# Kernel optimization log

Measured on AMD Instinct MI355X. Metric: run time of the kernel, lower is better.

Reference implementation:

```python
import jax, jax.numpy as jnp
import numpy as np

N = 500_000   # nodes
E = 16_000_000  # edges (avg degree 32)


def setup_inputs() -> dict:
    key = jax.random.key(0)
    ks = jax.random.split(key, 12)
    x = jax.random.normal(ks[0], (N, 1), dtype=jnp.float32)
    edge_index = jax.random.randint(ks[1], (2, E), 0, N, dtype=jnp.int32)
    # GCNConv weights: conv1(1->4), conv2(4->4), conv3(4->2), classifier Linear(2->1)
    def w(k, fin, fout):
        return jax.random.normal(k, (fin, fout), dtype=jnp.float32) / np.sqrt(fin)
    W1, b1 = w(ks[2], 1, 4), jnp.zeros((4,), jnp.float32)
    W2, b2 = w(ks[3], 4, 4), jnp.zeros((4,), jnp.float32)
    W3, b3 = w(ks[4], 4, 2), jnp.zeros((2,), jnp.float32)
    Wc, bc = w(ks[5], 2, 1), jnp.zeros((1,), jnp.float32)
    return {"x": x, "edge_index": edge_index, "W1": W1, "b1": b1,
            "W2": W2, "b2": b2, "W3": W3, "b3": b3, "Wc": Wc, "bc": bc}


def _gcn_conv(h, src, dst, dinv, W, b):
    # PyG GCNConv: out = D^{-1/2}(A+I)D^{-1/2} (h W) + b
    h = h @ W  # [N, Fout], tiny Fout so transform-first is cheapest
    norm = dinv[src] * dinv[dst]          # [E]
    msg = h[src] * norm[:, None]          # [E, Fout]
    agg = jax.ops.segment_sum(msg, dst, num_segments=N)
    # self-loop contribution: norm = dinv[i]^2
    agg = agg + h * (dinv * dinv)[:, None]
    return agg + b


def reference(x, edge_index, W1, b1, W2, b2, W3, b3, Wc, bc):
    src, dst = edge_index[0], edge_index[1]
    # degree including self-loop (count of incoming edges at dst, PyG gcn_norm)
    deg = jax.ops.segment_sum(jnp.ones((E,), jnp.float32), dst, num_segments=N) + 1.0
    dinv = jax.lax.rsqrt(deg)
    h = jnp.tanh(_gcn_conv(x, src, dst, dinv, W1, b1))
    h = jnp.tanh(_gcn_conv(h, src, dst, dinv, W2, b2))
    h = jnp.tanh(_gcn_conv(h, src, dst, dinv, W3, b3))
    out = h @ Wc + bc
    return (out, h)
```

## Files before the change

kernel.cpp:

```cpp
#include <hip/hip_runtime.h>

#define NN   500000
#define NE   16000000

#define NBUCK   245
#define NWGA    1000
#define CHUNKA4 4000
#define NBINB   1954
#define NWGB    2000
#define CHUNKB4 2000
#define CAP     14336

typedef int      vint4   __attribute__((ext_vector_type(4)));
typedef float    vfloat4 __attribute__((ext_vector_type(4)));
typedef float    vfloat2 __attribute__((ext_vector_type(2)));
typedef _Float16 vhalf4  __attribute__((ext_vector_type(4)));
typedef _Float16 vhalf2  __attribute__((ext_vector_type(2)));

__global__ __launch_bounds__(256) void hist_kernel(const int* __restrict__ dst,
                                                   int* __restrict__ wgHist,
                                                   int shift, int nbin, int chunk4) {
    __shared__ int hist[NBINB];
    for (int i = threadIdx.x; i < nbin; i += 256) hist[i] = 0;
    __syncthreads();
    const vint4* d4 = (const vint4*)(dst + (size_t)blockIdx.x * chunk4 * 4);
    for (int i = threadIdx.x; i < chunk4; i += 256) {
        vint4 d = __builtin_nontemporal_load(d4 + i);
        atomicAdd(&hist[d.x >> shift], 1);
        atomicAdd(&hist[d.y >> shift], 1);
        atomicAdd(&hist[d.z >> shift], 1);
        atomicAdd(&hist[d.w >> shift], 1);
    }
    __syncthreads();
    int* row = wgHist + (size_t)blockIdx.x * nbin;
    for (int i = threadIdx.x; i < nbin; i += 256) row[i] = hist[i];
}

__global__ __launch_bounds__(256) void scanbins_kernel(int* __restrict__ wgHist,
                                                       int* __restrict__ binTotal,
                                                       int nwg, int nbin) {
    __shared__ int partials[256];
    int bin = blockIdx.x;
    int t = threadIdx.x;
    int per = (nwg + 255) / 256;
    int w0 = t * per;
    int w1 = w0 + per; if (w1 > nwg) w1 = nwg;
    int s = 0;
    for (int w = w0; w < w1; ++w) s += wgHist[(size_t)w * nbin + bin];
    partials[t] = s;
    __syncthreads();
    if (t == 0) {
        int run = 0;
        for (int i = 0; i < 256; ++i) { int tmp = partials[i]; partials[i] = run; run += tmp; }
        binTotal[bin] = run;
    }
    __syncthreads();
    int off = partials[t];
    for (int w = w0; w < w1; ++w) {
        size_t idx = (size_t)w * nbin + bin;
        int v = wgHist[idx];
        wgHist[idx] = off;
        off += v;
    }
}

__global__ void scantotal_kernel(const int* __restrict__ binTotal, int* __restrict__ binStart,
                                 int nbin) {
    __shared__ int partials[512];
    int t = threadIdx.x;
    int base = t * 4;
    int v[4]; int s = 0;
#pragma unroll
    for (int j = 0; j < 4; ++j) {
        int b = base + j;
        v[j] = (b < nbin) ? binTotal[b] : 0;
        s += v[j];
    }
    partials[t] = s;
    __syncthreads();
    if (t == 0) {
        int run = 0;
        for (int i = 0; i < 512; ++i) { int tmp = partials[i]; partials[i] = run; run += tmp; }
        binStart[nbin] = run;
    }
    __syncthreads();
    int off = partials[t];
#pragma unroll
    for (int j = 0; j < 4; ++j) {
        int b = base + j;
        if (b < nbin) binStart[b] = off;
        off += v[j];
    }
}

__global__ __launch_bounds__(256) void reorder_kernel(const int* __restrict__ src,
                                                      const int* __restrict__ dst,
                                                      const int* __restrict__ wgHist,
                                                      const int* __restrict__ binStart,
                                                      int* __restrict__ outbuf,
                                                      int shift, int nbin, int chunk4) {
    __shared__ int cur[NBINB];
    const int* row = wgHist + (size_t)blockIdx.x * nbin;
    for (int i = threadIdx.x; i < nbin; i += 256) cur[i] = binStart[i] + row[i];
    __syncthreads();
    const int mask = (1 << shift) - 1;
    const vint4* s4 = (const vint4*)(src + (size_t)blockIdx.x * chunk4 * 4);
    const vint4* d4 = (const vint4*)(dst + (size_t)blockIdx.x * chunk4 * 4);
    for (int i = threadIdx.x; i < chunk4; i += 256) {
        vint4 s = __builtin_nontemporal_load(s4 + i);
        vint4 d = __builtin_nontemporal_load(d4 + i);
        int ss[4] = {s.x, s.y, s.z, s.w};
        int dd[4] = {d.x, d.y, d.z, d.w};
#pragma unroll
        for (int k = 0; k < 4; ++k) {
            int pos = atomicAdd(&cur[dd[k] >> shift], 1);
            outbuf[pos] = (ss[k] << shift) | (dd[k] & mask);
        }
    }
}

__global__ __launch_bounds__(512) void csr_kernel(const int* __restrict__ bktStart,
                                                  const int* __restrict__ bucketbuf,
                                                  int* __restrict__ edgebuf,
                                                  const float* __restrict__ x,
                                                  float* __restrict__ dinv,
                                                  float* __restrict__ p1,
                                                  int* __restrict__ rowStart) {
    __shared__ int cnt[2048];
    __shared__ int pref[2048];
    __shared__ int partials[512];
    int b = blockIdx.x, t = threadIdx.x;
    for (int k = t; k < 2048; k += 512) cnt[k] = 0;
    __syncthreads();
    int e0 = bktStart[b], e1 = bktStart[b + 1];
    int n = e1 - e0;
    for (int i = t; i < n; i += 512)
        atomicAdd(&cnt[bucketbuf[e0 + i] & 2047], 1);
    __syncthreads();
    int base = t * 4;
    int c0 = cnt[base], c1 = cnt[base + 1], c2 = cnt[base + 2], c3 = cnt[base + 3];
    partials[t] = c0 + c1 + c2 + c3;
    __syncthreads();
    if (t == 0) {
        int run = 0;
        for (int i = 0; i < 512; ++i) { int tmp = partials[i]; partials[i] = run; run += tmp; }
    }
    __syncthreads();
    int off = partials[t];
    int cc[4] = {c0, c1, c2, c3};
#pragma unroll
    for (int j = 0; j < 4; ++j) { pref[base + j] = off; off += cc[j]; }
#pragma unroll
    for (int j = 0; j < 4; ++j) {
        int k = base + j;
        int node = b * 2048 + k;
        if (node < NN) {
            rowStart[node] = e0 + pref[k];
            float di = rsqrtf((float)cc[j] + 1.0f);
            dinv[node] = di;
            p1[node] = x[node] * di;
        }
    }
    if (b == NBUCK - 1 && t == 0) rowStart[NN] = e1;
    __syncthreads();
#pragma unroll
    for (int j = 0; j < 4; ++j) { int k = base + j; cnt[k] = e0 + pref[k]; }
    __syncthreads();
    for (int i = t; i < n; i += 512) {
        int e = bucketbuf[e0 + i];
        int pos = atomicAdd(&cnt[e & 2047], 1);
        edgebuf[pos] = e >> 11;
    }
}

__global__ __launch_bounds__(256) void sortbin_kernel(const int* __restrict__ binStart,
                                                      int* __restrict__ edgebuf,
                                                      const float* __restrict__ x,
                                                      float* __restrict__ dinv,
                                                      float* __restrict__ p1,
                                                      int* __restrict__ rowStart) {
    __shared__ int stage[CAP];
    __shared__ int cnt[256];
    __shared__ int pref[256];
    __shared__ int cur[256];
    int b = blockIdx.x, t = threadIdx.x;
    cnt[t] = 0;
    __syncthreads();
    int e0 = binStart[b], e1 = binStart[b + 1];
    int n = e1 - e0;
    if (n > CAP) n = CAP;
    for (int i = t; i < n; i += 256) {
        int e = edgebuf[e0 + i];
        stage[i] = e;
        atomicAdd(&cnt[e & 255], 1);
    }
    __syncthreads();
    if (t == 0) {
        int run = 0;
        for (int i = 0; i < 256; ++i) { pref[i] = run; run += cnt[i]; }
    }
    __syncthreads();
    cur[t] = pref[t];
    int node = b * 256 + t;
    if (node < NN) {
        rowStart[node] = e0 + pref[t];
        float di = rsqrtf((float)cnt[t] + 1.0f);
        dinv[node] = di;
        p1[node] = x[node] * di;
    }
    if (b == NBINB - 1 && t == 0) rowStart[NN] = binStart[NBINB];
    __syncthreads();
    for (int i = t; i < n; i += 256) {
        int e = stage[i];
        int pos = e0 + atomicAdd(&cur[e & 255], 1);
        edgebuf[pos] = e >> 8;
    }
}

__global__ __launch_bounds__(256) void agg1_kernel(const int* __restrict__ rowStart,
                                                   const int* __restrict__ edgebuf,
                                                   const float* __restrict__ p1,
                                                   const float* __restrict__ dinv,
                                                   const float* __restrict__ W1,
                                                   const float* __restrict__ b1,
                                                   const float* __restrict__ W2,
                                                   vhalf4* __restrict__ p2h) {
    int node = blockIdx.x * blockDim.x + threadIdx.x;
    if (node >= NN) return;
    int r0 = rowStart[node], r1 = rowStart[node + 1];
    float s0 = 0.f, s1 = 0.f, s2 = 0.f, s3 = 0.f;
    float s4 = 0.f, s5 = 0.f, s6 = 0.f, s7 = 0.f;
    int k = r0;
    for (; k + 8 <= r1; k += 8) {
        int a = edgebuf[k],     b = edgebuf[k + 1];
        int c = edgebuf[k + 2], d = edgebuf[k + 3];
        int e = edgebuf[k + 4], f = edgebuf[k + 5];
        int g = edgebuf[k + 6], h = edgebuf[k + 7];
        s0 += p1[a]; s1 += p1[b]; s2 += p1[c]; s3 += p1[d];
        s4 += p1[e]; s5 += p1[f]; s6 += p1[g]; s7 += p1[h];
    }
    for (; k < r1; ++k) s0 += p1[edgebuf[k]];
    float acc = ((s0 + s1) + (s2 + s3)) + ((s4 + s5) + (s6 + s7));
    float di = dinv[node];
    float t = di * (acc + p1[node]);
    float h1[4];
#pragma unroll
    for (int f2 = 0; f2 < 4; ++f2) h1[f2] = tanhf(t * W1[f2] + b1[f2]);
    vhalf4 g;
    g.x = (_Float16)(di * (h1[0]*W2[0] + h1[1]*W2[4] + h1[2]*W2[8]  + h1[3]*W2[12]));
    g.y = (_Float16)(di * (h1[0]*W2[1] + h1[1]*W2[5] + h1[2]*W2[9]  + h1[3]*W2[13]));
    g.z = (_Float16)(di * (h1[0]*W2[2] + h1[1]*W2[6] + h1[2]*W2[10] + h1[3]*W2[14]));
    g.w = (_Float16)(di * (h1[0]*W2[3] + h1[1]*W2[7] + h1[2]*W2[11] + h1[3]*W2[15]));
    p2h[node] = g;
}

__global__ __launch_bounds__(256) void agg2_kernel(const int* __restrict__ rowStart,
                                                   const int* __restrict__ edgebuf,
                                                   const vhalf4* __restrict__ p2h,
                                                   const float* __restrict__ dinv,
                                                   const float* __restrict__ b2,
                                                   const float* __restrict__ W3,
                                                   vhalf2* __restrict__ p3h) {
    int node = blockIdx.x * blockDim.x + threadIdx.x;
    if (node >= NN) return;
    int r0 = rowStart[node], r1 = rowStart[node + 1];
    vfloat4 sA = {0.f, 0.f, 0.f, 0.f};
    vfloat4 sB = {0.f, 0.f, 0.f, 0.f};
    vfloat4 sC = {0.f, 0.f, 0.f, 0.f};
    vfloat4 sD = {0.f, 0.f, 0.f, 0.f};
    int k = r0;
    for (; k + 8 <= r1; k += 8) {
        int a = edgebuf[k],     b = edgebuf[k + 1];
        int c = edgebuf[k + 2], d = edgebuf[k + 3];
        int e = edgebuf[k + 4], f = edgebuf[k + 5];
        int g = edgebuf[k + 6], h = edgebuf[k + 7];
        vhalf4 qa = p2h[a], qb = p2h[b], qc = p2h[c], qd = p2h[d];
        vhalf4 qe = p2h[e], qf = p2h[f], qg = p2h[g], qh = p2h[h];
        sA.x += (float)qa.x + (float)qb.x; sB.x += (float)qc.x + (float)qd.x;
        sA.y += (float)qa.y + (float)qb.y; sB.y += (float)qc.y + (float)qd.y;
        sA.z += (float)qa.z + (float)qb.z; sB.z += (float)qc.z + (float)qd.z;
        sA.w += (float)qa.w + (float)qb.w; sB.w += (float)qc.w + (float)qd.w;
        sC.x += (float)qe.x + (float)qf.x; sD.x += (float)qg.x + (float)qh.x;
        sC.y += (float)qe.y + (float)qf.y; sD.y += (float)qg.y + (float)qh.y;
        sC.z += (float)qe.z + (float)qf.z; sD.z += (float)qg.z + (float)qh.z;
        sC.w += (float)qe.w + (float)qf.w; sD.w += (float)qg.w + (float)qh.w;
    }
    for (; k < r1; ++k) {
        vhalf4 q = p2h[edgebuf[k]];
        sA.x += (float)q.x; sA.y += (float)q.y; sA.z += (float)q.z; sA.w += (float)q.w;
    }
    float di = dinv[node];
    vhalf4 pw = p2h[node];
    float h2[4];
    h2[0] = tanhf(di * (sA.x + sB.x + sC.x + sD.x + (float)pw.x) + b2[0]);
    h2[1] = tanhf(di * (sA.y + sB.y + sC.y + sD.y + (float)pw.y) + b2[1]);
    h2[2] = tanhf(di * (sA.z + sB.z + sC.z + sD.z + (float)pw.z) + b2[2]);
    h2[3] = tanhf(di * (sA.w + sB.w + sC.w + sD.w + (float)pw.w) + b2[3]);
    vhalf2 o;
    o.x = (_Float16)(di * (h2[0]*W3[0] + h2[1]*W3[2] + h2[2]*W3[4] + h2[3]*W3[6]));
    o.y = (_Float16)(di * (h2[0]*W3[1] + h2[1]*W3[3] + h2[2]*W3[5] + h2[3]*W3[7]));
    p3h[node] = o;
}

__global__ __launch_bounds__(256) void agg3_kernel(const int* __restrict__ rowStart,
                                                   const int* __restrict__ edgebuf,
                                                   const vhalf2* __restrict__ p3h,
                                                   const float* __restrict__ dinv,
                                                   const float* __restrict__ b3,
                                                   const float* __restrict__ Wc,
                                                   const float* __restrict__ bc,
                                                   float* __restrict__ out) {
    int node = blockIdx.x * blockDim.x + threadIdx.x;
    if (node >= NN) return;
    int r0 = rowStart[node], r1 = rowStart[node + 1];
    float ax = 0.f, ay = 0.f, bx = 0.f, by = 0.f;
    float cx = 0.f, cy = 0.f, dx = 0.f, dy = 0.f;
    int k = r0;
    for (; k + 8 <= r1; k += 8) {
        int a = edgebuf[k],     b = edgebuf[k + 1];
        int c = edgebuf[k + 2], d = edgebuf[k + 3];
        int e = edgebuf[k + 4], f = edgebuf[k + 5];
        int g = edgebuf[k + 6], h = edgebuf[k + 7];
        vhalf2 qa = p3h[a], qb = p3h[b], qc = p3h[c], qd = p3h[d];
        vhalf2 qe = p3h[e], qf = p3h[f], qg = p3h[g], qh = p3h[h];
        ax += (float)qa.x + (float)qb.x; bx += (float)qc.x + (float)qd.x;
        ay += (float)qa.y + (float)qb.y; by += (float)qc.y + (float)qd.y;
        cx += (float)qe.x + (float)qf.x; dx += (float)qg.x + (float)qh.x;
        cy += (float)qe.y + (float)qf.y; dy += (float)qg.y + (float)qh.y;
    }
    for (; k < r1; ++k) {
        vhalf2 q = p3h[edgebuf[k]];
        ax += (float)q.x; ay += (float)q.y;
    }
    float di = dinv[node];
    vhalf2 pw = p3h[node];
    float h0 = tanhf(di * (ax + bx + cx + dx + (float)pw.x) + b3[0]);
    float h1 = tanhf(di * (ay + by + cy + dy + (float)pw.y) + b3[1]);
    __builtin_nontemporal_store(h0 * Wc[0] + h1 * Wc[1] + bc[0], out + node);
    vfloat2 hh; hh.x = h0; hh.y = h1;
    __builtin_nontemporal_store(hh, (vfloat2*)(out + NN) + node);
}


extern "C" void kernel_launch(void* const* d_in, const int* in_sizes, int n_in,
                              void* d_out, int out_size, void* d_ws, size_t ws_size,
                              hipStream_t stream) {
    const float* x   = (const float*)d_in[0];
    const int*   ei  = (const int*)d_in[1];
    const float* W1  = (const float*)d_in[2];
    const float* b1  = (const float*)d_in[3];
    const float* W2  = (const float*)d_in[4];
    const float* b2  = (const float*)d_in[5];
    const float* W3  = (const float*)d_in[6];
    const float* b3  = (const float*)d_in[7];
    const float* Wc  = (const float*)d_in[8];
    const float* bc  = (const float*)d_in[9];
    float* out = (float*)d_out;
    float* ws  = (float*)d_ws;

    const int* src = ei;
    const int* dst = ei + NE;

    float*  dinv     = ws;
    float*  p1       = ws + (size_t)NN;
    vhalf4* p2h      = (vhalf4*)(ws + 2ull * NN);
    vhalf2* p3h      = (vhalf2*)(ws + 4ull * NN);
    int*    rowStart = (int*)(ws + 5ull * NN);
    int*    tail     = (int*)(ws + 6ull * NN + 1);

    const int B = 256;
    const int aggGrid = (NN + B - 1) / B;

    const size_t needA = (6ull * NN + 1 + (size_t)NWGA * NBUCK + NBUCK + NBUCK + 1
                          + 2ull * NE) * 4ull;

    if (ws_size >= needA) {
        int* wgHist    = tail;
        int* bktTotal  = wgHist + (size_t)NWGA * NBUCK;
        int* bktStart  = bktTotal + NBUCK;
        int* bucketbuf = bktStart + NBUCK + 1;
        int* edgebuf   = bucketbuf + (size_t)NE;

        hipLaunchKernelGGL(hist_kernel, dim3(NWGA), dim3(B), 0, stream,
                           dst, wgHist, 11, NBUCK, CHUNKA4);
        hipLaunchKernelGGL(scanbins_kernel, dim3(NBUCK), dim3(B), 0, stream,
                           wgHist, bktTotal, NWGA, NBUCK);
        hipLaunchKernelGGL(scantotal_kernel, dim3(1), dim3(512), 0, stream,
                           bktTotal, bktStart, NBUCK);
        hipLaunchKernelGGL(reorder_kernel, dim3(NWGA), dim3(B), 0, stream,
                           src, dst, wgHist, bktStart, bucketbuf, 11, NBUCK, CHUNKA4);
        hipLaunchKernelGGL(csr_kernel, dim3(NBUCK), dim3(512), 0, stream,
                           bktStart, bucketbuf, edgebuf, x, dinv, p1, rowStart);
        hipLaunchKernelGGL(agg1_kernel, dim3(aggGrid), dim3(B), 0, stream,
                           rowStart, edgebuf, p1, dinv, W1, b1, W2, p2h);
        hipLaunchKernelGGL(agg2_kernel, dim3(aggGrid), dim3(B), 0, stream,
                           rowStart, edgebuf, p2h, dinv, b2, W3, p3h);
        hipLaunchKernelGGL(agg3_kernel, dim3(aggGrid), dim3(B), 0, stream,
                           rowStart, edgebuf, p3h, dinv, b3, Wc, bc, out);
    } else {
        int* wgHist   = tail;
        int* binTotal = wgHist + (size_t)NWGB * NBINB;
        int* binStart = binTotal + NBINB;
        int* edgebuf  = binStart + NBINB + 1;

        hipLaunchKernelGGL(hist_kernel, dim3(NWGB), dim3(B), 0, stream,
                           dst, wgHist, 8, NBINB, CHUNKB4);
        hipLaunchKernelGGL(scanbins_kernel, dim3(NBINB), dim3(B), 0, stream,
                           wgHist, binTotal, NWGB, NBINB);
        hipLaunchKernelGGL(scantotal_kernel, dim3(1), dim3(512), 0, stream,
                           binTotal, binStart, NBINB);
        hipLaunchKernelGGL(reorder_kernel, dim3(NWGB), dim3(B), 0, stream,
                           src, dst, wgHist, binStart, edgebuf, 8, NBINB, CHUNKB4);
        hipLaunchKernelGGL(sortbin_kernel, dim3(NBINB), dim3(B), 0, stream,
                           binStart, edgebuf, x, dinv, p1, rowStart);
        hipLaunchKernelGGL(agg1_kernel, dim3(aggGrid), dim3(B), 0, stream,
                           rowStart, edgebuf, p1, dinv, W1, b1, W2, p2h);
        hipLaunchKernelGGL(agg2_kernel, dim3(aggGrid), dim3(B), 0, stream,
                           rowStart, edgebuf, p2h, dinv, b2, W3, p3h);
        hipLaunchKernelGGL(agg3_kernel, dim3(aggGrid), dim3(B), 0, stream,
                           rowStart, edgebuf, p3h, dinv, b3, Wc, bc, out);
    }
}
```

Before: 738.9 us.

## Split per-bucket CSR build into sub-bin partition plus per-bin sort

Replaces the 245-block csr_kernel, which did a 2048-way shared-memory counting sort per bucket, with two passes. A subbin kernel partitions each bucket into 8 sub-bins of 256 nodes using wave-aggregated ballot atomics. The existing sortbin kernel then finishes the sort with 1954 blocks. This aims to raise parallelism beyond 245 workgroups and cut LDS atomic contention, at the cost of an extra full pass over the 16M-entry edge buffer and one more launch.

```diff
diff --git a/kernel.cpp b/kernel.cpp
--- a/kernel.cpp
+++ b/kernel.cpp
@@ -2,11 +2,11 @@
 
 #define NN   500000
 #define NE   16000000
+#define NBIN 1954
 
 #define NBUCK   245
 #define NWGA    1000
 #define CHUNKA4 4000
-#define NBINB   1954
 #define NWGB    2000
 #define CHUNKB4 2000
 #define CAP     14336
@@ -20,7 +20,7 @@
 __global__ __launch_bounds__(256) void hist_kernel(const int* __restrict__ dst,
                                                    int* __restrict__ wgHist,
                                                    int shift, int nbin, int chunk4) {
-    __shared__ int hist[NBINB];
+    __shared__ int hist[NBIN];
     for (int i = threadIdx.x; i < nbin; i += 256) hist[i] = 0;
     __syncthreads();
     const vint4* d4 = (const vint4*)(dst + (size_t)blockIdx.x * chunk4 * 4);
@@ -99,7 +99,7 @@
                                                       const int* __restrict__ binStart,
                                                       int* __restrict__ outbuf,
                                                       int shift, int nbin, int chunk4) {
-    __shared__ int cur[NBINB];
+    __shared__ int cur[NBIN];
     const int* row = wgHist + (size_t)blockIdx.x * nbin;
     for (int i = threadIdx.x; i < nbin; i += 256) cur[i] = binStart[i] + row[i];
     __syncthreads();
@@ -119,57 +119,57 @@
     }
 }
 
-__global__ __launch_bounds__(512) void csr_kernel(const int* __restrict__ bktStart,
-                                                  const int* __restrict__ bucketbuf,
-                                                  int* __restrict__ edgebuf,
-                                                  const float* __restrict__ x,
-                                                  float* __restrict__ dinv,
-                                                  float* __restrict__ p1,
-                                                  int* __restrict__ rowStart) {
-    __shared__ int cnt[2048];
-    __shared__ int pref[2048];
-    __shared__ int partials[512];
+__global__ __launch_bounds__(512) void subbin_kernel(const int* __restrict__ bktStart,
+                                                     const int* __restrict__ bucketbuf,
+                                                     int* __restrict__ binbuf,
+                                                     int* __restrict__ sbStart) {
+    __shared__ int cnt8[8];
+    __shared__ int cur8[8];
     int b = blockIdx.x, t = threadIdx.x;
-    for (int k = t; k < 2048; k += 512) cnt[k] = 0;
+    int bin0 = b * 8;
+    int nsub = NBIN - bin0; if (nsub > 8) nsub = 8;
+    if (t < 8) cnt8[t] = 0;
     __syncthreads();
     int e0 = bktStart[b], e1 = bktStart[b + 1];
-    int n = e1 - e0;
-    for (int i = t; i < n; i += 512)
-        atomicAdd(&cnt[bucketbuf[e0 + i] & 2047], 1);
-    __syncthreads();
-    int base = t * 4;
-    int c0 = cnt[base], c1 = cnt[base + 1], c2 = cnt[base + 2], c3 = cnt[base + 3];
-    partials[t] = c0 + c1 + c2 + c3;
+    int lane = t & 63;
+    for (int i = e0 + t; i < e1; i += 512) {
+        int sub = (bucketbuf[i] & 2047) >> 8;
+#pragma unroll
+        for (int j = 0; j < 8; ++j) {
+            unsigned long long m = __ballot(sub == j);
+            if (sub == j && lane == (int)__ffsll(m) - 1)
+                atomicAdd(&cnt8[j], (int)__popcll(m));
+        }
+    }
     __syncthreads();
     if (t == 0) {
-        int run = 0;
-        for (int i = 0; i < 512; ++i) { int tmp = partials[i]; partials[i] = run; run += tmp; }
-    }
-    __syncthreads();
-    int off = partials[t];
-    int cc[4] = {c0, c1, c2, c3};
-#pragma unroll
-    for (int j = 0; j < 4; ++j) { pref[base + j] = off; off += cc[j]; }
-#pragma unroll
-    for (int j = 0; j < 4; ++j) {
-        int k = base + j;
-        int node = b * 2048 + k;
-        if (node < NN) {
-            rowStart[node] = e0 + pref[k];
-            float di = rsqrtf((float)cc[j] + 1.0f);
-            dinv[node] = di;
-            p1[node] = x[node] * di;
+        int run = e0;
+#pragma unroll
+        for (int j = 0; j < 8; ++j) {
+            cur8[j] = run;
+            if (j < nsub) sbStart[bin0 + j] = run;
+            run += cnt8[j];
         }
     }
-    if (b == NBUCK - 1 && t == 0) rowStart[NN] = e1;
-    __syncthreads();
-#pragma unroll
-    for (int j = 0; j < 4; ++j) { int k = base + j; cnt[k] = e0 + pref[k]; }
-    __syncthreads();
-    for (int i = t; i < n; i += 512) {
-        int e = bucketbuf[e0 + i];
-        int pos = atomicAdd(&cnt[e & 2047], 1);
-        edgebuf[pos] = e >> 11;
+    if (b == NBUCK - 1 && t == 64) sbStart[NBIN] = e1;
+    __syncthreads();
+    for (int i = e0 + t; i < e1; i += 512) {
+        int e = bucketbuf[i];
+        int sub = (e & 2047) >> 8;
+        int pk = ((e >> 11) << 8) | (e & 255);
+        int pos = 0;
+#pragma unroll
+        for (int j = 0; j < 8; ++j) {
+            unsigned long long m = __ballot(sub == j);
+            if (sub == j) {
+                int leader = (int)__ffsll(m) - 1;
+                int base;
+                if (lane == leader) base = atomicAdd(&cur8[j], (int)__popcll(m));
+                base = __shfl(base, leader);
+                pos = base + (int)__popcll(m & ((1ull << lane) - 1ull));
+            }
+        }
+        binbuf[pos] = pk;
     }
 }
 
@@ -208,7 +208,7 @@
         dinv[node] = di;
         p1[node] = x[node] * di;
     }
-    if (b == NBINB - 1 && t == 0) rowStart[NN] = binStart[NBINB];
+    if (b == NBIN - 1 && t == 0) rowStart[NN] = binStart[NBIN];
     __syncthreads();
     for (int i = t; i < n; i += 256) {
         int e = stage[i];
@@ -372,14 +372,15 @@
     const int aggGrid = (NN + B - 1) / B;
 
     const size_t needA = (6ull * NN + 1 + (size_t)NWGA * NBUCK + NBUCK + NBUCK + 1
-                          + 2ull * NE) * 4ull;
+                          + NBIN + 1 + 2ull * NE) * 4ull;
 
     if (ws_size >= needA) {
         int* wgHist    = tail;
         int* bktTotal  = wgHist + (size_t)NWGA * NBUCK;
         int* bktStart  = bktTotal + NBUCK;
-        int* bucketbuf = bktStart + NBUCK + 1;
-        int* edgebuf   = bucketbuf + (size_t)NE;
+        int* sbStart   = bktStart + NBUCK + 1;
+        int* bucketbuf = sbStart + NBIN + 1;
+        int* binbuf    = bucketbuf + (size_t)NE;
 
         hipLaunchKernelGGL(hist_kernel, dim3(NWGA), dim3(B), 0, stream,
                            dst, wgHist, 11, NBUCK, CHUNKA4);
@@ -389,29 +390,31 @@
                            bktTotal, bktStart, NBUCK);
         hipLaunchKernelGGL(reorder_kernel, dim3(NWGA), dim3(B), 0, stream,
                            src, dst, wgHist, bktStart, bucketbuf, 11, NBUCK, CHUNKA4);
-        hipLaunchKernelGGL(csr_kernel, dim3(NBUCK), dim3(512), 0, stream,
-                           bktStart, bucketbuf, edgebuf, x, dinv, p1, rowStart);
+        hipLaunchKernelGGL(subbin_kernel, dim3(NBUCK), dim3(512), 0, stream,
+                           bktStart, bucketbuf, binbuf, sbStart);
+        hipLaunchKernelGGL(sortbin_kernel, dim3(NBIN), dim3(B), 0, stream,
+                           sbStart, binbuf, x, dinv, p1, rowStart);
         hipLaunchKernelGGL(agg1_kernel, dim3(aggGrid), dim3(B), 0, stream,
-                           rowStart, edgebuf, p1, dinv, W1, b1, W2, p2h);
+                           rowStart, binbuf, p1, dinv, W1, b1, W2, p2h);
         hipLaunchKernelGGL(agg2_kernel, dim3(aggGrid), dim3(B), 0, stream,
-                           rowStart, edgebuf, p2h, dinv, b2, W3, p3h);
+                           rowStart, binbuf, p2h, dinv, b2, W3, p3h);
         hipLaunchKernelGGL(agg3_kernel, dim3(aggGrid), dim3(B), 0, stream,
-                           rowStart, edgebuf, p3h, dinv, b3, Wc, bc, out);
+                           rowStart, binbuf, p3h, dinv, b3, Wc, bc, out);
     } else {
         int* wgHist   = tail;
-        int* binTotal = wgHist + (size_t)NWGB * NBINB;
-        int* binStart = binTotal + NBINB;
-        int* edgebuf  = binStart + NBINB + 1;
+        int* binTotal = wgHist + (size_t)NWGB * NBIN;
+        int* binStart = binTotal + NBIN;
+        int* edgebuf  = binStart + NBIN + 1;
 
         hipLaunchKernelGGL(hist_kernel, dim3(NWGB), dim3(B), 0, stream,
-                           dst, wgHist, 8, NBINB, CHUNKB4);
-        hipLaunchKernelGGL(scanbins_kernel, dim3(NBINB), dim3(B), 0, stream,
-                           wgHist, binTotal, NWGB, NBINB);
+                           dst, wgHist, 8, NBIN, CHUNKB4);
+        hipLaunchKernelGGL(scanbins_kernel, dim3(NBIN), dim3(B), 0, stream,
+                           wgHist, binTotal, NWGB, NBIN);
         hipLaunchKernelGGL(scantotal_kernel, dim3(1), dim3(512), 0, stream,
-                           binTotal, binStart, NBINB);
+                           binTotal, binStart, NBIN);
         hipLaunchKernelGGL(reorder_kernel, dim3(NWGB), dim3(B), 0, stream,
-                           src, dst, wgHist, binStart, edgebuf, 8, NBINB, CHUNKB4);
-        hipLaunchKernelGGL(sortbin_kernel, dim3(NBINB), dim3(B), 0, stream,
+                           src, dst, wgHist, binStart, edgebuf, 8, NBIN, CHUNKB4);
+        hipLaunchKernelGGL(sortbin_kernel, dim3(NBIN), dim3(B), 0, stream,
                            binStart, edgebuf, x, dinv, p1, rowStart);
         hipLaunchKernelGGL(agg1_kernel, dim3(aggGrid), dim3(B), 0, stream,
                            rowStart, edgebuf, p1, dinv, W1, b1, W2, p2h);
```

Result: slower. 955.2 us (+29.3%).
